# Optimization experiments

Hardware: AMD Instinct MI355X
Metric: run time of the kernel (lower is better)

## Reference

```python
import jax, jax.numpy as jnp
import numpy as np

# Binarize (sign) with straight-through estimator, matching the BNN-style
# BinarizeConv2d which replaces .data in-place (identity gradient path).
@jax.custom_vjp
def binarize(x):
    return jnp.where(x >= 0, 1.0, -1.0).astype(x.dtype)

def _bin_fwd(x):
    return binarize(x), None

def _bin_bwd(_, g):
    return (g,)

binarize.defvjp(_bin_fwd, _bin_bwd)

def conv2d(x, w, pad):
    # x: NCHW, w: OIHW, stride 1, symmetric 'same' padding for odd kernels
    return jax.lax.conv_general_dilated(
        x, w, window_strides=(1, 1), padding=[(pad, pad), (pad, pad)],
        dimension_numbers=("NCHW", "OIHW", "NCHW"))

def batchnorm2d(x, gamma, beta, eps=1e-5):
    # training-mode BatchNorm2d: batch statistics over (N, H, W)
    mean = jnp.mean(x, axis=(0, 2, 3), keepdims=True)
    var = jnp.var(x, axis=(0, 2, 3), keepdims=True)
    inv = gamma[None, :, None, None] * jax.lax.rsqrt(var + eps)
    return (x - mean) * inv + beta[None, :, None, None]

def leaky_relu(x, slope=0.5):
    return jnp.where(x >= 0, x, slope * x)

def setup_inputs() -> dict:
    key = jax.random.key(0)
    ks = jax.random.split(key, 4)
    B, H, W = 16, 256, 256
    x = jax.random.normal(ks[0], (B, 1, H, W), dtype=jnp.float32)
    w1 = jax.random.normal(ks[1], (128, 1, 7, 7), dtype=jnp.float32) * 0.1
    w2 = jax.random.normal(ks[2], (64, 128, 1, 1), dtype=jnp.float32) * 0.1
    w3 = jax.random.normal(ks[3], (1, 64, 5, 5), dtype=jnp.float32) * 0.05
    g1 = jnp.ones((128,), jnp.float32)
    b1 = jnp.zeros((128,), jnp.float32)
    g2 = jnp.ones((64,), jnp.float32)
    b2 = jnp.zeros((64,), jnp.float32)
    return {"x": x, "w1": w1, "g1": g1, "b1": b1,
            "w2": w2, "g2": g2, "b2": b2, "w3": w3}

def reference(x, w1, g1, b1, w2, g2, b2, w3):
    # layer1: binarized conv (in=1 channel != 3 -> input also binarized) + BN + LeakyReLU(0.5)
    h = conv2d(binarize(x), binarize(w1), pad=3)
    h = leaky_relu(batchnorm2d(h, g1, b1))
    # layer2: binarized 1x1 conv + BN + LeakyReLU(0.5)
    h = conv2d(binarize(h), binarize(w2), pad=0)
    h = leaky_relu(batchnorm2d(h, g2, b2))
    # layer3: plain full-precision 5x5 conv, no bias
    return conv2d(h, w3, pad=2)
```

## Files before the change

### kernel.cpp

```cpp
#include <hip/hip_runtime.h>
#include <cstdint>
#include <cstddef>
#include <climits>


#define NPIX_PER_CH (16.0 * 256.0 * 256.0)
#define PLANE_BYTES 67584
#define ROW_BYTES   264
#define FXSCALE     262144.0f
#define FXINV       3.814697265625e-06f

typedef _Float16 half2_t __attribute__((ext_vector_type(2)));

#if __has_builtin(__builtin_amdgcn_fdot2)
__device__ __forceinline__ float DOT2(half2_t a, half2_t b, float c) {
    return __builtin_amdgcn_fdot2(a, b, c, false);
}
#else
__device__ __forceinline__ float DOT2(half2_t a, half2_t b, float c) {
    return fmaf((float)a[0], (float)b[0], fmaf((float)a[1], (float)b[1], c));
}
#endif

__device__ __forceinline__ uint32_t pk_f16(float lo, float hi) {
#if __has_builtin(__builtin_amdgcn_cvt_pkrtz)
    auto h = __builtin_amdgcn_cvt_pkrtz(lo, hi);
    return __builtin_bit_cast(uint32_t, h);
#else
    half2_t h; h[0] = (_Float16)lo; h[1] = (_Float16)hi;
    return __builtin_bit_cast(uint32_t, h);
#endif
}
#define H2(u) __builtin_bit_cast(half2_t, (uint32_t)(u))

struct WS {
    int8_t*   h2s;
    uint64_t* xbits;
    uint64_t* wb1;
    uint64_t* w2lo;
    uint64_t* w2hi;
    long long* st1;
    long long* st2;
    int*      K1;
    unsigned long long* flipm;
    float* a2; float* c2;
    uint32_t* wtab;
};

static inline WS carve(void* d_ws) {
    WS w;
    uint8_t* p = (uint8_t*)d_ws;
    w.h2s   = (int8_t*)p;              p += (size_t)16 * 64 * PLANE_BYTES;
    w.xbits = (uint64_t*)p;            p += (size_t)16 * 256 * 6 * 8;
    w.wb1   = (uint64_t*)p;            p += 128 * 8;
    w.w2lo  = (uint64_t*)p;            p += 64 * 8;
    w.w2hi  = (uint64_t*)p;            p += 64 * 8;
    w.st1   = (long long*)p;           p += 256 * 8;
    w.st2   = (long long*)p;           p += 128 * 8;
    w.K1    = (int*)p;                 p += 128 * 4;
    w.flipm = (unsigned long long*)p;  p += 2 * 8;
    w.a2    = (float*)p;               p += 64 * 4;
    w.c2    = (float*)p;               p += 64 * 4;
    w.wtab  = (uint32_t*)p;            p += 64 * 32 * 4;
    return w;
}

__global__ __launch_bounds__(256) void k_pack_x(const float* __restrict__ x,
                                                uint64_t* __restrict__ xbits) {
    int rowId = blockIdx.x * 4 + (threadIdx.x >> 6);
    int lane  = threadIdx.x & 63;
    const float* row = x + (size_t)rowId * 256;
    uint64_t b0 = __ballot(row[0 * 64 + lane] < 0.0f);
    uint64_t b1 = __ballot(row[1 * 64 + lane] < 0.0f);
    uint64_t b2 = __ballot(row[2 * 64 + lane] < 0.0f);
    uint64_t b3 = __ballot(row[3 * 64 + lane] < 0.0f);
    if (lane == 0) {
        uint64_t* o = xbits + (size_t)rowId * 6;
        o[0] = b0 << 8;
        o[1] = (b0 >> 56) | (b1 << 8);
        o[2] = (b1 >> 56) | (b2 << 8);
        o[3] = (b2 >> 56) | (b3 << 8);
        o[4] = b3 >> 56;
        o[5] = 0;
    }
}

__global__ void k_pack_w(const float* __restrict__ w1, const float* __restrict__ w2,
                         uint64_t* __restrict__ wb1, uint64_t* __restrict__ w2lo,
                         uint64_t* __restrict__ w2hi,
                         long long* __restrict__ st1, long long* __restrict__ st2) {
    int t = threadIdx.x;
    if (t < 128) {
        uint64_t b = 0;
        for (int k = 0; k < 49; ++k)
            if (w1[t * 49 + k] < 0.0f) b |= (1ull << k);
        wb1[t] = b;
    } else if (t < 192) {
        int o = t - 128;
        uint64_t lo = 0, hi = 0;
        for (int c = 0; c < 64; ++c) if (w2[o * 128 + c]      < 0.0f) lo |= (1ull << c);
        for (int c = 0; c < 64; ++c) if (w2[o * 128 + 64 + c] < 0.0f) hi |= (1ull << c);
        w2lo[o] = lo; w2hi[o] = hi;
    }
    st1[t] = 0;
    if (t < 128) st2[t] = 0;
}

__device__ inline void build_window(const uint64_t* __restrict__ xb_img, int y, int x,
                                    uint64_t& sbits, uint64_t& vmask) {
    int bitpos = x + 5;
    int w  = bitpos >> 6;
    int sh = bitpos & 63;
    int lo = 3 - x;   if (lo < 0) lo = 0;
    int hi = 258 - x; if (hi > 6) hi = 6;
    uint64_t hm = ((1ull << (hi - lo + 1)) - 1ull) << lo;
    sbits = 0; vmask = 0;
    #pragma unroll
    for (int dy = 0; dy < 7; ++dy) {
        int yy = y - 3 + dy;
        if (yy < 0 || yy > 255) continue;
        const uint64_t* r = xb_img + (size_t)yy * 6;
        uint64_t wA = r[w], wB = r[w + 1];
        uint64_t bits = wA >> sh;
        if (sh) bits |= wB << (64 - sh);
        bits &= 0x7Full;
        sbits |= bits << (7 * dy);
        vmask |= hm   << (7 * dy);
    }
}

__global__ __launch_bounds__(256) void k_stats1(const uint64_t* __restrict__ xbits,
                                                const uint64_t* __restrict__ wb1g,
                                                long long* __restrict__ st1) {
    __shared__ uint64_t sb[256];
    __shared__ uint64_t vm[256];
    __shared__ int rs[128];
    __shared__ int rq[128];
    int t = threadIdx.x;
    int c = t & 127, half = t >> 7;
    uint64_t wb = wb1g[c];
    int sum = 0;
    int sumsq = 0;
    for (int row = blockIdx.x; row < 4096; row += gridDim.x) {
        int n = row >> 8, y = row & 255;
        const uint64_t* xb_img = xbits + (size_t)n * 256 * 6;
        uint64_t s, v;
        build_window(xb_img, y, t, s, v);
        sb[t] = s; vm[t] = v;
        __syncthreads();
        int base = half << 7;
        auto edge = [&](int p) {
            uint64_t vv = vm[base + p];
            uint64_t d = (sb[base + p] ^ wb) & vv;
            int h = __popcll(vv) - 2 * __popcll(d);
            sum += h; sumsq += h * h;
        };
        if (y >= 3 && y <= 252) {
            int lo = (half == 0) ? 3 : 0;
            int hi = (half == 0) ? 128 : 125;
            for (int p = 0; p < lo; ++p) edge(p);
            #pragma unroll 4
            for (int p = lo; p < hi; ++p) {
                uint64_t d = sb[base + p] ^ wb;
                int h = 49 - 2 * __popcll(d);
                sum += h; sumsq += h * h;
            }
            for (int p = hi; p < 128; ++p) edge(p);
        } else {
            #pragma unroll 4
            for (int p = 0; p < 128; ++p) edge(p);
        }
        __syncthreads();
    }
    if (half == 1) { rs[c] = sum; rq[c] = sumsq; }
    __syncthreads();
    if (half == 0) {
        long long S = (long long)sum + rs[c];
        long long Q = (long long)sumsq + rq[c];
        atomicAdd((unsigned long long*)&st1[c],       (unsigned long long)S);
        atomicAdd((unsigned long long*)&st1[128 + c], (unsigned long long)Q);
    }
}

__global__ void k_fin1(const long long* __restrict__ st1,
                       const float* __restrict__ g1, const float* __restrict__ b1,
                       int* __restrict__ K1, unsigned long long* __restrict__ flipm) {
    int c = threadIdx.x;
    double mean = (double)st1[c] / NPIX_PER_CH;
    double var  = (double)st1[128 + c] / NPIX_PER_CH - mean * mean;
    double a = (double)g1[c] / sqrt(var + 1e-5);
    double cst = (double)b1[c] - mean * a;
    int K; int flip = 0;
    if (a > 0.0) {
        double v = -cst / a;
        v = fmin(fmax(v, -100.0), 100.0);
        K = (int)ceil(v);
    } else if (a < 0.0) {
        double v = -cst / a;
        v = fmin(fmax(v, -100.0), 100.0);
        K = (int)floor(v) + 1; flip = 1;
    } else {
        K = INT_MIN; flip = (cst < 0.0) ? 1 : 0;
    }
    K1[c] = K;
    unsigned long long m = __ballot(flip != 0);
    if ((c & 63) == 0) flipm[c >> 6] = m;
}

__global__ __launch_bounds__(256) void k_conv2(const uint64_t* __restrict__ xbits,
                                               const uint64_t* __restrict__ wb1g,
                                               const int* __restrict__ K1g,
                                               const unsigned long long* __restrict__ flipm,
                                               const uint64_t* __restrict__ w2log,
                                               const uint64_t* __restrict__ w2hig,
                                               int8_t* __restrict__ h2s) {
    __shared__ uint64_t wb1s[128];
    __shared__ int      K1s[128];
    __shared__ uint64_t w2l[64], w2h[64];
    int t = threadIdx.x;
    if (t < 128) { wb1s[t] = wb1g[t]; K1s[t] = K1g[t]; }
    else if (t < 192) { int o = t - 128; w2l[o] = w2log[o]; w2h[o] = w2hig[o]; }
    __syncthreads();

    int idx = blockIdx.x * 256 + t;
    int n = idx >> 16, rem = idx & 65535;
    int y = rem >> 8, x = rem & 255;
    const uint64_t* xb_img = xbits + (size_t)n * 256 * 6;
    uint64_t sbits, vmask;
    build_window(xb_img, y, x, sbits, vmask);
    int nv = __popcll(vmask);

    uint64_t blo = 0, bhi = 0;
    #pragma unroll 8
    for (int cc = 0; cc < 64; ++cc) {
        uint64_t d = (sbits ^ wb1s[cc]) & vmask;
        int h = nv - 2 * __popcll(d);
        blo |= (uint64_t)(h < K1s[cc]) << cc;
    }
    #pragma unroll 8
    for (int cc = 0; cc < 64; ++cc) {
        uint64_t d = (sbits ^ wb1s[64 + cc]) & vmask;
        int h = nv - 2 * __popcll(d);
        bhi |= (uint64_t)(h < K1s[64 + cc]) << cc;
    }
    blo ^= flipm[0];
    bhi ^= flipm[1];

    size_t base = (size_t)(n * 64) * PLANE_BYTES + (size_t)y * ROW_BYTES;
    #pragma unroll 8
    for (int o = 0; o < 64; ++o) {
        int m = __popcll(blo ^ w2l[o]) + __popcll(bhi ^ w2h[o]);
        h2s[base + (size_t)o * PLANE_BYTES + 2 + x] = (int8_t)(64 - m);
    }
    if (x == 0) {
        #pragma unroll 8
        for (int o = 0; o < 64; ++o)
            *(short*)(h2s + base + (size_t)o * PLANE_BYTES) = 0;
    }
    if (x == 255) {
        #pragma unroll 8
        for (int o = 0; o < 64; ++o) {
            int8_t* r = h2s + base + (size_t)o * PLANE_BYTES;
            *(short*)(r + 258) = 0;
            *(int*)(r + 260) = 0;
        }
    }
}

__global__ __launch_bounds__(256) void k_stats2(const int8_t* __restrict__ h2s,
                                                long long* __restrict__ st2) {
    int plane = blockIdx.x;
    int o = plane & 63;
    int t = threadIdx.x;
    const int4* p = (const int4*)(h2s + (size_t)plane * PLANE_BYTES);
    int sum = 0, sumsq = 0;
    for (int si = t; si < 4224; si += 256) {
        int4 v4 = p[si];
        int wv[4] = {v4.x, v4.y, v4.z, v4.w};
        #pragma unroll
        for (int j = 0; j < 4; ++j) {
            #pragma unroll
            for (int k = 0; k < 4; ++k) {
                int b = (int)(int8_t)((unsigned)wv[j] >> (8 * k));
                sum += b;
                sumsq += b * b;
            }
        }
    }
    for (int off = 32; off; off >>= 1) {
        sum   += __shfl_down(sum, off);
        sumsq += __shfl_down(sumsq, off);
    }
    __shared__ int ws1[4], ws2[4];
    int wid = t >> 6;
    if ((t & 63) == 0) { ws1[wid] = sum; ws2[wid] = sumsq; }
    __syncthreads();
    if (t == 0) {
        long long S = 0, Q = 0;
        for (int i = 0; i < 4; ++i) { S += ws1[i]; Q += ws2[i]; }
        atomicAdd((unsigned long long*)&st2[o],      (unsigned long long)S);
        atomicAdd((unsigned long long*)&st2[64 + o], (unsigned long long)Q);
    }
}

__global__ void k_fin2(const long long* __restrict__ st2,
                       const float* __restrict__ g2, const float* __restrict__ b2,
                       const float* __restrict__ w3,
                       float* __restrict__ a2, float* __restrict__ c2,
                       uint32_t* __restrict__ wtab) {
    int o = threadIdx.x;
    double mean = 2.0 * (double)st2[o] / NPIX_PER_CH;
    double msq  = 4.0 * (double)st2[64 + o] / NPIX_PER_CH;
    double var  = msq - mean * mean;
    double inv  = (double)g2[o] / sqrt(var + 1e-5);
    a2[o] = (float)(2.0 * inv);
    c2[o] = (float)((double)b2[o] - mean * inv);

    uint32_t* wp = wtab + o * 32;
    #pragma unroll
    for (int dy = 0; dy < 5; ++dy) {
        float w0 = w3[o * 25 + dy * 5 + 0];
        float w1 = w3[o * 25 + dy * 5 + 1];
        float w2v = w3[o * 25 + dy * 5 + 2];
        float w3v = w3[o * 25 + dy * 5 + 3];
        float w4 = w3[o * 25 + dy * 5 + 4];
        half2_t h;
        h[0] = (_Float16)w0;  h[1] = (_Float16)w1;  wp[dy*6+0] = __builtin_bit_cast(uint32_t, h);
        h[0] = (_Float16)w2v; h[1] = (_Float16)w3v; wp[dy*6+1] = __builtin_bit_cast(uint32_t, h);
        h[0] = (_Float16)w4;  h[1] = (_Float16)0.f; wp[dy*6+2] = __builtin_bit_cast(uint32_t, h);
        h[0] = (_Float16)0.f; h[1] = (_Float16)w0;  wp[dy*6+3] = __builtin_bit_cast(uint32_t, h);
        h[0] = (_Float16)w1;  h[1] = (_Float16)w2v; wp[dy*6+4] = __builtin_bit_cast(uint32_t, h);
        h[0] = (_Float16)w3v; h[1] = (_Float16)w4;  wp[dy*6+5] = __builtin_bit_cast(uint32_t, h);
    }
    wp[30] = 0; wp[31] = 0;
}

__global__ __launch_bounds__(256) void k_zero3(int4* __restrict__ o) {
    int i = blockIdx.x * 256 + threadIdx.x;
    #pragma unroll
    for (int j = 0; j < 4; ++j)
        o[(size_t)i * 4 + j] = make_int4(0, 0, 0, 0);
}

__global__ __launch_bounds__(256, 4) void k_conv3(const int8_t* __restrict__ h2s,
                                                  const float* __restrict__ a2g,
                                                  const float* __restrict__ c2g,
                                                  const uint32_t* __restrict__ wtab,
                                                  int* __restrict__ outi) {
    __shared__ uint16_t lds[4 * 36 * 72];
    __shared__ float sA2[16], sC2[16];
    int t = threadIdx.x;
    int bid = blockIdx.x;
    int cg   = bid >> 9;
    int rest = bid & 511;
    int n  = rest >> 5;
    int yt = (rest >> 2) & 7;
    int xt = rest & 3;
    int ty0 = yt * 32, tx0 = xt * 64;
    int cgbase = cg * 16;
    if (t < 16) { sA2[t] = a2g[cgbase + t]; sC2[t] = c2g[cgbase + t]; }

    int ty = t >> 4, tx = t & 15;
    int n64 = n * 64;

    float acc[2][4] = {{0.f,0.f,0.f,0.f},{0.f,0.f,0.f,0.f}};

    for (int kk = 0; kk < 4; ++kk) {
        __syncthreads();
        for (int si = t; si < 2448; si += 256) {
            int cl  = si / 612;
            int rem = si - cl * 612;
            int row = rem / 17;
            int q   = rem - row * 17;
            int gy  = ty0 - 2 + row;
            int lc  = 4 * kk + cl;
            float a = sA2[lc], c = sC2[lc];
            uint32_t u0 = 0, u1 = 0;
            if ((unsigned)gy < 256u) {
                int v = *(const int*)(h2s + (size_t)(n64 + cgbase + lc) * PLANE_BYTES
                                          + (size_t)gy * ROW_BYTES + tx0 + q * 4);
                float z0 = fmaf(a, (float)(int)(int8_t)(v),        c);
                float z1 = fmaf(a, (float)(int)(int8_t)(v >> 8),   c);
                float z2 = fmaf(a, (float)(int)(int8_t)(v >> 16),  c);
                float z3 = fmaf(a, (float)(int)(int8_t)(v >> 24),  c);
                z0 = fmaxf(z0, 0.5f * z0);
                z1 = fmaxf(z1, 0.5f * z1);
                z2 = fmaxf(z2, 0.5f * z2);
                z3 = fmaxf(z3, 0.5f * z3);
                u0 = pk_f16(z0, z1);
                u1 = pk_f16(z2, z3);
            }
            uint2 wv = {u0, u1};
            *(uint2*)(lds + cl * 2592 + row * 72 + q * 4) = wv;
        }
        __syncthreads();

        #pragma unroll
        for (int cl = 0; cl < 4; ++cl) {
            const uint32_t* wp = wtab + (size_t)(cgbase + 4 * kk + cl) * 32;
            const uint16_t* base = lds + cl * 2592 + (2 * ty) * 72 + 4 * tx;
            uint2 A[6], B[6];
            #pragma unroll
            for (int rr = 0; rr < 6; ++rr) {
                A[rr] = *(const uint2*)(base + rr * 72);
                B[rr] = *(const uint2*)(base + rr * 72 + 4);
            }
            #pragma unroll
            for (int rr = 0; rr < 6; ++rr) {
                half2_t W0 = H2(A[rr].x), W1 = H2(A[rr].y);
                half2_t W2 = H2(B[rr].x), W3 = H2(B[rr].y);
                #pragma unroll
                for (int dyp = rr - 1; dyp <= rr; ++dyp) {
                    if (dyp < 0 || dyp > 4) continue;
                    int r = rr - dyp;
                    const uint32_t* wd = wp + dyp * 6;
                    acc[r][0] = DOT2(W0, H2(wd[0]), DOT2(W1, H2(wd[1]), DOT2(W2, H2(wd[2]), acc[r][0])));
                    acc[r][1] = DOT2(W0, H2(wd[3]), DOT2(W1, H2(wd[4]), DOT2(W2, H2(wd[5]), acc[r][1])));
                    acc[r][2] = DOT2(W1, H2(wd[0]), DOT2(W2, H2(wd[1]), DOT2(W3, H2(wd[2]), acc[r][2])));
                    acc[r][3] = DOT2(W1, H2(wd[3]), DOT2(W2, H2(wd[4]), DOT2(W3, H2(wd[5]), acc[r][3])));
                }
            }
        }
    }

    int ox = tx0 + 4 * tx;
    #pragma unroll
    for (int r = 0; r < 2; ++r) {
        int oy = ty0 + 2 * ty + r;
        size_t o = (size_t)n * 65536 + (size_t)oy * 256 + ox;
        #pragma unroll
        for (int j = 0; j < 4; ++j) {
            int q = __float2int_rn(acc[r][j] * FXSCALE);
            atomicAdd(outi + o + j, q);
        }
    }
}

__global__ __launch_bounds__(256) void k_fin3(int* __restrict__ o) {
    int i = blockIdx.x * 256 + threadIdx.x;
    int4 v = ((const int4*)o)[i];
    float4 f = {v.x * FXINV, v.y * FXINV, v.z * FXINV, v.w * FXINV};
    ((float4*)o)[i] = f;
}

extern "C" void kernel_launch(void* const* d_in, const int* in_sizes, int n_in,
                              void* d_out, int out_size, void* d_ws, size_t ws_size,
                              hipStream_t stream) {
    const float* x  = (const float*)d_in[0];
    const float* w1 = (const float*)d_in[1];
    const float* g1 = (const float*)d_in[2];
    const float* b1 = (const float*)d_in[3];
    const float* w2 = (const float*)d_in[4];
    const float* g2 = (const float*)d_in[5];
    const float* b2 = (const float*)d_in[6];
    const float* w3 = (const float*)d_in[7];

    WS ws = carve(d_ws);

    k_zero3<<<256, 256, 0, stream>>>((int4*)d_out);
    k_pack_x<<<1024, 256, 0, stream>>>(x, ws.xbits);
    k_pack_w<<<1, 256, 0, stream>>>(w1, w2, ws.wb1, ws.w2lo, ws.w2hi, ws.st1, ws.st2);
    k_stats1<<<1024, 256, 0, stream>>>(ws.xbits, ws.wb1, ws.st1);
    k_fin1<<<1, 128, 0, stream>>>(ws.st1, g1, b1, ws.K1, ws.flipm);
    k_conv2<<<4096, 256, 0, stream>>>(ws.xbits, ws.wb1, ws.K1, ws.flipm,
                                      ws.w2lo, ws.w2hi, ws.h2s);
    k_stats2<<<1024, 256, 0, stream>>>(ws.h2s, ws.st2);
    k_fin2<<<1, 64, 0, stream>>>(ws.st2, g2, b2, w3, ws.a2, ws.c2, ws.wtab);
    k_conv3<<<2048, 256, 0, stream>>>(ws.h2s, ws.a2, ws.c2, ws.wtab, (int*)d_out);
    k_fin3<<<1024, 256, 0, stream>>>((int*)d_out);
}
```

Before: 244.1 us.

## Register-block stats1 channels, uniform-load weights in conv2, prefetch h2s in conv3

k_stats1 now has each thread handle 4 channels across 32 pixels, reusing each shared-memory window load four times, and reduces partial sums with wave shuffles instead of an LDS pass. k_conv2 drops its LDS staging and barrier and reads packed weight/threshold records (uint4) directly from global memory with block-uniform indices, so they can go through scalar loads. k_conv3 precomputes its staging addresses and software-prefetches the next channel group's int8 tiles into registers while the current group is being convolved. The cost is higher register pressure in all three kernels.

```diff
diff --git a/kernel.cpp b/kernel.cpp
--- a/kernel.cpp
+++ b/kernel.cpp
@@ -39,9 +39,10 @@
     uint64_t* wb1;
     uint64_t* w2lo;
     uint64_t* w2hi;
+    uint4*    w2pk;
     long long* st1;
     long long* st2;
-    int*      K1;
+    uint4*    pk1;
     unsigned long long* flipm;
     float* a2; float* c2;
     uint32_t* wtab;
@@ -55,9 +56,10 @@
     w.wb1   = (uint64_t*)p;            p += 128 * 8;
     w.w2lo  = (uint64_t*)p;            p += 64 * 8;
     w.w2hi  = (uint64_t*)p;            p += 64 * 8;
+    w.w2pk  = (uint4*)p;               p += 64 * 16;
     w.st1   = (long long*)p;           p += 256 * 8;
     w.st2   = (long long*)p;           p += 128 * 8;
-    w.K1    = (int*)p;                 p += 128 * 4;
+    w.pk1   = (uint4*)p;               p += 128 * 16;
     w.flipm = (unsigned long long*)p;  p += 2 * 8;
     w.a2    = (float*)p;               p += 64 * 4;
     w.c2    = (float*)p;               p += 64 * 4;
@@ -87,7 +89,7 @@
 
 __global__ void k_pack_w(const float* __restrict__ w1, const float* __restrict__ w2,
                          uint64_t* __restrict__ wb1, uint64_t* __restrict__ w2lo,
-                         uint64_t* __restrict__ w2hi,
+                         uint64_t* __restrict__ w2hi, uint4* __restrict__ w2pk,
                          long long* __restrict__ st1, long long* __restrict__ st2) {
     int t = threadIdx.x;
     if (t < 128) {
@@ -101,6 +103,8 @@
         for (int c = 0; c < 64; ++c) if (w2[o * 128 + c]      < 0.0f) lo |= (1ull << c);
         for (int c = 0; c < 64; ++c) if (w2[o * 128 + 64 + c] < 0.0f) hi |= (1ull << c);
         w2lo[o] = lo; w2hi[o] = hi;
+        w2pk[o] = make_uint4((uint32_t)lo, (uint32_t)(lo >> 32),
+                             (uint32_t)hi, (uint32_t)(hi >> 32));
     }
     st1[t] = 0;
     if (t < 128) st2[t] = 0;
@@ -134,13 +138,15 @@
                                                 long long* __restrict__ st1) {
     __shared__ uint64_t sb[256];
     __shared__ uint64_t vm[256];
-    __shared__ int rs[128];
-    __shared__ int rq[128];
     int t = threadIdx.x;
-    int c = t & 127, half = t >> 7;
-    uint64_t wb = wb1g[c];
-    int sum = 0;
-    int sumsq = 0;
+    int g = t >> 3, pg = t & 7;
+    uint64_t wb[4];
+    #pragma unroll
+    for (int i = 0; i < 4; ++i) wb[i] = wb1g[4 * g + i];
+    int sum[4] = {0, 0, 0, 0};
+    int sq[4]  = {0, 0, 0, 0};
+    int p0 = 32 * pg;
+
     for (int row = blockIdx.x; row < 4096; row += gridDim.x) {
         int n = row >> 8, y = row & 255;
         const uint64_t* xb_img = xbits + (size_t)n * 256 * 6;
@@ -148,43 +154,49 @@
         build_window(xb_img, y, t, s, v);
         sb[t] = s; vm[t] = v;
         __syncthreads();
-        int base = half << 7;
-        auto edge = [&](int p) {
-            uint64_t vv = vm[base + p];
-            uint64_t d = (sb[base + p] ^ wb) & vv;
-            int h = __popcll(vv) - 2 * __popcll(d);
-            sum += h; sumsq += h * h;
-        };
-        if (y >= 3 && y <= 252) {
-            int lo = (half == 0) ? 3 : 0;
-            int hi = (half == 0) ? 128 : 125;
-            for (int p = 0; p < lo; ++p) edge(p);
-            #pragma unroll 4
-            for (int p = lo; p < hi; ++p) {
-                uint64_t d = sb[base + p] ^ wb;
-                int h = 49 - 2 * __popcll(d);
-                sum += h; sumsq += h * h;
+        bool iy = (y >= 3 && y <= 252);
+        #pragma unroll 4
+        for (int j = 0; j < 32; ++j) {
+            int p = p0 + j;
+            uint64_t ss = sb[p];
+            if (iy && p >= 3 && p <= 252) {
+                #pragma unroll
+                for (int i = 0; i < 4; ++i) {
+                    int h = 49 - 2 * __popcll(ss ^ wb[i]);
+                    sum[i] += h; sq[i] += h * h;
+                }
+            } else {
+                uint64_t vv = vm[p];
+                int nvp = __popcll(vv);
+                #pragma unroll
+                for (int i = 0; i < 4; ++i) {
+                    int h = nvp - 2 * __popcll((ss ^ wb[i]) & vv);
+                    sum[i] += h; sq[i] += h * h;
+                }
             }
-            for (int p = hi; p < 128; ++p) edge(p);
-        } else {
-            #pragma unroll 4
-            for (int p = 0; p < 128; ++p) edge(p);
         }
         __syncthreads();
     }
-    if (half == 1) { rs[c] = sum; rq[c] = sumsq; }
-    __syncthreads();
-    if (half == 0) {
-        long long S = (long long)sum + rs[c];
-        long long Q = (long long)sumsq + rq[c];
-        atomicAdd((unsigned long long*)&st1[c],       (unsigned long long)S);
-        atomicAdd((unsigned long long*)&st1[128 + c], (unsigned long long)Q);
+    #pragma unroll
+    for (int i = 0; i < 4; ++i) {
+        sum[i] += __shfl_xor(sum[i], 1); sum[i] += __shfl_xor(sum[i], 2); sum[i] += __shfl_xor(sum[i], 4);
+        sq[i]  += __shfl_xor(sq[i], 1);  sq[i]  += __shfl_xor(sq[i], 2);  sq[i]  += __shfl_xor(sq[i], 4);
+    }
+    if (pg == 0) {
+        #pragma unroll
+        for (int i = 0; i < 4; ++i) {
+            atomicAdd((unsigned long long*)&st1[4 * g + i],
+                      (unsigned long long)(long long)sum[i]);
+            atomicAdd((unsigned long long*)&st1[128 + 4 * g + i],
+                      (unsigned long long)(long long)sq[i]);
+        }
     }
 }
 
 __global__ void k_fin1(const long long* __restrict__ st1,
                        const float* __restrict__ g1, const float* __restrict__ b1,
-                       int* __restrict__ K1, unsigned long long* __restrict__ flipm) {
+                       const uint64_t* __restrict__ wb1,
+                       uint4* __restrict__ pk1, unsigned long long* __restrict__ flipm) {
     int c = threadIdx.x;
     double mean = (double)st1[c] / NPIX_PER_CH;
     double var  = (double)st1[128 + c] / NPIX_PER_CH - mean * mean;
@@ -202,54 +214,49 @@
     } else {
         K = INT_MIN; flip = (cst < 0.0) ? 1 : 0;
     }
-    K1[c] = K;
+    uint64_t wb = wb1[c];
+    pk1[c] = make_uint4((uint32_t)wb, (uint32_t)(wb >> 32), (uint32_t)K, 0u);
     unsigned long long m = __ballot(flip != 0);
     if ((c & 63) == 0) flipm[c >> 6] = m;
 }
 
 __global__ __launch_bounds__(256) void k_conv2(const uint64_t* __restrict__ xbits,
-                                               const uint64_t* __restrict__ wb1g,
-                                               const int* __restrict__ K1g,
+                                               const uint4* __restrict__ pk1,
                                                const unsigned long long* __restrict__ flipm,
-                                               const uint64_t* __restrict__ w2log,
-                                               const uint64_t* __restrict__ w2hig,
+                                               const uint4* __restrict__ w2pk,
                                                int8_t* __restrict__ h2s) {
-    __shared__ uint64_t wb1s[128];
-    __shared__ int      K1s[128];
-    __shared__ uint64_t w2l[64], w2h[64];
     int t = threadIdx.x;
-    if (t < 128) { wb1s[t] = wb1g[t]; K1s[t] = K1g[t]; }
-    else if (t < 192) { int o = t - 128; w2l[o] = w2log[o]; w2h[o] = w2hig[o]; }
-    __syncthreads();
-
-    int idx = blockIdx.x * 256 + t;
-    int n = idx >> 16, rem = idx & 65535;
-    int y = rem >> 8, x = rem & 255;
+    int n = blockIdx.x >> 8, y = blockIdx.x & 255, x = t;
     const uint64_t* xb_img = xbits + (size_t)n * 256 * 6;
     uint64_t sbits, vmask;
     build_window(xb_img, y, x, sbits, vmask);
     int nv = __popcll(vmask);
 
     uint64_t blo = 0, bhi = 0;
-    #pragma unroll 8
+    #pragma unroll 16
     for (int cc = 0; cc < 64; ++cc) {
-        uint64_t d = (sbits ^ wb1s[cc]) & vmask;
-        int h = nv - 2 * __popcll(d);
-        blo |= (uint64_t)(h < K1s[cc]) << cc;
-    }
-    #pragma unroll 8
+        uint4 pk = pk1[cc];
+        uint64_t wb = ((uint64_t)pk.y << 32) | pk.x;
+        int h = nv - 2 * __popcll((sbits ^ wb) & vmask);
+        blo |= (uint64_t)(h < (int)pk.z) << cc;
+    }
+    #pragma unroll 16
     for (int cc = 0; cc < 64; ++cc) {
-        uint64_t d = (sbits ^ wb1s[64 + cc]) & vmask;
-        int h = nv - 2 * __popcll(d);
-        bhi |= (uint64_t)(h < K1s[64 + cc]) << cc;
+        uint4 pk = pk1[64 + cc];
+        uint64_t wb = ((uint64_t)pk.y << 32) | pk.x;
+        int h = nv - 2 * __popcll((sbits ^ wb) & vmask);
+        bhi |= (uint64_t)(h < (int)pk.z) << cc;
     }
     blo ^= flipm[0];
     bhi ^= flipm[1];
 
+    uint32_t b0 = (uint32_t)blo, b1 = (uint32_t)(blo >> 32);
+    uint32_t b2 = (uint32_t)bhi, b3 = (uint32_t)(bhi >> 32);
     size_t base = (size_t)(n * 64) * PLANE_BYTES + (size_t)y * ROW_BYTES;
-    #pragma unroll 8
+    #pragma unroll 16
     for (int o = 0; o < 64; ++o) {
-        int m = __popcll(blo ^ w2l[o]) + __popcll(bhi ^ w2h[o]);
+        uint4 w = w2pk[o];
+        int m = __popc(b0 ^ w.x) + __popc(b1 ^ w.y) + __popc(b2 ^ w.z) + __popc(b3 ^ w.w);
         h2s[base + (size_t)o * PLANE_BYTES + 2 + x] = (int8_t)(64 - m);
     }
     if (x == 0) {
@@ -361,24 +368,42 @@
     if (t < 16) { sA2[t] = a2g[cgbase + t]; sC2[t] = c2g[cgbase + t]; }
 
     int ty = t >> 4, tx = t & 15;
-    int n64 = n * 64;
+    int pbase = n * 64 + cgbase;
+
+    int s_cl[10], s_lds[10];
+    const int8_t* s_ptr[10];
+    bool s_has[10], s_ok[10];
+    #pragma unroll
+    for (int it = 0; it < 10; ++it) {
+        int si = t + 256 * it;
+        int cl  = si / 612;
+        int rem = si - cl * 612;
+        int row = rem / 17;
+        int q   = rem - row * 17;
+        int gy  = ty0 - 2 + row;
+        bool has = (si < 2448);
+        bool ok  = has && ((unsigned)gy < 256u);
+        s_cl[it]  = cl;
+        s_lds[it] = cl * 2592 + row * 72 + q * 4;
+        s_ptr[it] = h2s + (size_t)(pbase + (has ? cl : 0)) * PLANE_BYTES
+                        + (size_t)(ok ? gy : 0) * ROW_BYTES + tx0 + q * 4;
+        s_has[it] = has; s_ok[it] = ok;
+    }
+    int vv[10];
+    #pragma unroll
+    for (int it = 0; it < 10; ++it)
+        vv[it] = s_ok[it] ? *(const int*)s_ptr[it] : 0;
 
     float acc[2][4] = {{0.f,0.f,0.f,0.f},{0.f,0.f,0.f,0.f}};
 
     for (int kk = 0; kk < 4; ++kk) {
         __syncthreads();
-        for (int si = t; si < 2448; si += 256) {
-            int cl  = si / 612;
-            int rem = si - cl * 612;
-            int row = rem / 17;
-            int q   = rem - row * 17;
-            int gy  = ty0 - 2 + row;
-            int lc  = 4 * kk + cl;
-            float a = sA2[lc], c = sC2[lc];
-            uint32_t u0 = 0, u1 = 0;
-            if ((unsigned)gy < 256u) {
-                int v = *(const int*)(h2s + (size_t)(n64 + cgbase + lc) * PLANE_BYTES
-                                          + (size_t)gy * ROW_BYTES + tx0 + q * 4);
+        #pragma unroll
+        for (int it = 0; it < 10; ++it) {
+            if (s_has[it]) {
+                int lc = 4 * kk + s_cl[it];
+                float a = sA2[lc], c = sC2[lc];
+                int v = vv[it];
                 float z0 = fmaf(a, (float)(int)(int8_t)(v),        c);
                 float z1 = fmaf(a, (float)(int)(int8_t)(v >> 8),   c);
                 float z2 = fmaf(a, (float)(int)(int8_t)(v >> 16),  c);
@@ -387,13 +412,18 @@
                 z1 = fmaxf(z1, 0.5f * z1);
                 z2 = fmaxf(z2, 0.5f * z2);
                 z3 = fmaxf(z3, 0.5f * z3);
-                u0 = pk_f16(z0, z1);
-                u1 = pk_f16(z2, z3);
+                uint2 wv2 = {pk_f16(z0, z1), pk_f16(z2, z3)};
+                *(uint2*)(lds + s_lds[it]) = wv2;
             }
-            uint2 wv = {u0, u1};
-            *(uint2*)(lds + cl * 2592 + row * 72 + q * 4) = wv;
         }
         __syncthreads();
+        if (kk < 3) {
+            #pragma unroll
+            for (int it = 0; it < 10; ++it) {
+                s_ptr[it] += 4 * PLANE_BYTES;
+                vv[it] = s_ok[it] ? *(const int*)s_ptr[it] : 0;
+            }
+        }
 
         #pragma unroll
         for (int cl = 0; cl < 4; ++cl) {
@@ -459,11 +489,11 @@
 
     k_zero3<<<256, 256, 0, stream>>>((int4*)d_out);
     k_pack_x<<<1024, 256, 0, stream>>>(x, ws.xbits);
-    k_pack_w<<<1, 256, 0, stream>>>(w1, w2, ws.wb1, ws.w2lo, ws.w2hi, ws.st1, ws.st2);
+    k_pack_w<<<1, 256, 0, stream>>>(w1, w2, ws.wb1, ws.w2lo, ws.w2hi, ws.w2pk,
+                                    ws.st1, ws.st2);
     k_stats1<<<1024, 256, 0, stream>>>(ws.xbits, ws.wb1, ws.st1);
-    k_fin1<<<1, 128, 0, stream>>>(ws.st1, g1, b1, ws.K1, ws.flipm);
-    k_conv2<<<4096, 256, 0, stream>>>(ws.xbits, ws.wb1, ws.K1, ws.flipm,
-                                      ws.w2lo, ws.w2hi, ws.h2s);
+    k_fin1<<<1, 128, 0, stream>>>(ws.st1, g1, b1, ws.wb1, ws.pk1, ws.flipm);
+    k_conv2<<<4096, 256, 0, stream>>>(ws.xbits, ws.pk1, ws.flipm, ws.w2pk, ws.h2s);
     k_stats2<<<1024, 256, 0, stream>>>(ws.h2s, ws.st2);
     k_fin2<<<1, 64, 0, stream>>>(ws.st2, g2, b2, w3, ws.a2, ws.c2, ws.wtab);
     k_conv3<<<2048, 256, 0, stream>>>(ws.h2s, ws.a2, ws.c2, ws.wtab, (int*)d_out);
```

After: 289.0 us. +18.4%, slower.
